# Kernel tuning notes

Measured on AMD Instinct MI355X. Metric: run time of the kernel, lower is better.

The kernel has to match this reference:

```python
import jax, jax.numpy as jnp
import numpy as np

V, D, H, L, E, DH, K, PMAX = 50257, 128, 4, 4, 8, 512, 2, 256
B, T = 8, 256


def setup_inputs() -> dict:
    key = jax.random.key(0)
    ks = jax.random.split(key, 10)
    s = 0.02
    def n(k, shape):
        return jax.random.normal(k, shape, jnp.float32) * s
    return dict(
        idx=jax.random.randint(ks[0], (B, T), 0, V),
        tok_emb=n(ks[1], (V, D)),
        pos_emb=n(ks[2], (PMAX, D)),
        ln1_g=jnp.ones((L, D), jnp.float32), ln1_b=jnp.zeros((L, D), jnp.float32),
        in_w=n(ks[3], (L, 3 * D, D)), in_b=jnp.zeros((L, 3 * D), jnp.float32),
        out_w=n(ks[4], (L, D, D)), out_b=jnp.zeros((L, D), jnp.float32),
        ln2_g=jnp.ones((L, D), jnp.float32), ln2_b=jnp.zeros((L, D), jnp.float32),
        gate_w=n(ks[5], (L, E, D)),
        w1=n(ks[6], (L, E, DH, D)),
        w2=n(ks[7], (L, E, D, DH)),
        lnf_g=jnp.ones((D,), jnp.float32), lnf_b=jnp.zeros((D,), jnp.float32),
        lm_w=n(ks[8], (V, D)),
    )


def _ln(x, g, b):
    mu = x.mean(-1, keepdims=True)
    var = jnp.var(x, -1, keepdims=True)
    return (x - mu) / jnp.sqrt(var + 1e-5) * g + b


def _moe(x, gw, w1, w2):
    # x: [N, D]; top-2 sparse MoE, computed densely per expert then combined.
    logits = x @ gw.T                              # [N, E]
    probs = jax.nn.softmax(logits, -1)
    topw, topi = jax.lax.top_k(probs, K)           # [N, K]
    topw = topw / topw.sum(-1, keepdims=True)
    we = (topw[..., None] * jax.nn.one_hot(topi, E, dtype=x.dtype)).sum(1)  # [N, E]
    h = jax.nn.silu(jnp.einsum('nd,ehd->neh', x, w1))   # [N, E, DH]
    y = jnp.einsum('neh,edh->ned', h, w2)               # [N, E, D]
    return jnp.einsum('ned,ne->nd', y, we)


def reference(idx, tok_emb, pos_emb, ln1_g, ln1_b, in_w, in_b, out_w, out_b,
              ln2_g, ln2_b, gate_w, w1, w2, lnf_g, lnf_b, lm_w):
    b, t = idx.shape
    x = tok_emb[idx] + pos_emb[:t]                 # [B, T, D]
    dh = D // H
    scale = 1.0 / np.sqrt(dh)
    for l in range(L):
        xl = _ln(x, ln1_g[l], ln1_b[l])
        qkv = xl @ in_w[l].T + in_b[l]
        q, k, v = jnp.split(qkv, 3, -1)
        q = q.reshape(b, t, H, dh)
        k = k.reshape(b, t, H, dh)
        v = v.reshape(b, t, H, dh)
        att = jax.nn.softmax(jnp.einsum('bqhd,bkhd->bhqk', q, k) * scale, -1)
        o = jnp.einsum('bhqk,bkhd->bqhd', att, v).reshape(b, t, D)
        x = x + o @ out_w[l].T + out_b[l]
        x2 = _ln(x, ln2_g[l], ln2_b[l]).reshape(b * t, D)
        x = x + _moe(x2, gate_w[l], w1[l], w2[l]).reshape(b, t, D)
    return _ln(x, lnf_g, lnf_b) @ lm_w.T           # [B, T, V]
```

## Files before the change

kernel.cpp:

```cpp
#include <hip/hip_runtime.h>
#include <math.h>

#define NTOK 2048
#define DD   128
#define NHEAD 4
#define DHEAD 32
#define NLAYER 4
#define NEXP 8
#define DHID 512
#define NVOCAB 50257
#define VPAD  50304
#define SEQ   256
#define NBATCH 8

typedef __attribute__((ext_vector_type(8))) short short8v;
typedef __attribute__((ext_vector_type(4))) float f32x4;

__device__ __forceinline__ unsigned short nm_bf16r(float f) {
  unsigned u = __float_as_uint(f);
  u += 0x7fffu + ((u >> 16) & 1u);
  return (unsigned short)(u >> 16);
}

__device__ __forceinline__ float nm_silu(float a) {
// ... 8 lines not shown
  float sx = 0.f, sy = 0.f, sz = 0.f, sw = 0.f;
#pragma unroll 16
  for (int k = 0; k < N4; ++k) {
    float4 av = a4[k], wv = w4[k];
    sx = fmaf(av.x, wv.x, sx);
    sy = fmaf(av.y, wv.y, sy);
    sz = fmaf(av.z, wv.z, sz);
    sw = fmaf(av.w, wv.w, sw);
  }
  return (sx + sy) + (sz + sw);
}

__global__ void nm_embed_ln(const int* __restrict__ idx, const float* __restrict__ tok,
                            const float* __restrict__ pos, const float* __restrict__ g,
                            const float* __restrict__ b, float* __restrict__ x,
                            float* __restrict__ xl) {
  int n = blockIdx.x, lane = threadIdx.x;
  int t = idx[n];
  float v0 = tok[(size_t)t * DD + lane]      + pos[(n % SEQ) * DD + lane];
  float v1 = tok[(size_t)t * DD + lane + 64] + pos[(n % SEQ) * DD + lane + 64];
  x[n * DD + lane]      = v0;
  x[n * DD + lane + 64] = v1;
  float s = v0 + v1;
#pragma unroll
  for (int o = 32; o > 0; o >>= 1) s += __shfl_xor(s, o, 64);
  float mu = s * (1.f / 128.f);
  float d0 = v0 - mu, d1 = v1 - mu;
  float q = d0 * d0 + d1 * d1;
#pragma unroll
  for (int o = 32; o > 0; o >>= 1) q += __shfl_xor(q, o, 64);
  float rstd = rsqrtf(q * (1.f / 128.f) + 1e-5f);
  xl[n * DD + lane]      = d0 * rstd * g[lane]      + b[lane];
  xl[n * DD + lane + 64] = d1 * rstd * g[lane + 64] + b[lane + 64];
}

__global__ void nm_ln(const float* __restrict__ in, const float* __restrict__ g,
                      const float* __restrict__ b, float* __restrict__ out) {
  int n = blockIdx.x, lane = threadIdx.x;
  float v0 = in[n * DD + lane], v1 = in[n * DD + lane + 64];
  float s = v0 + v1;
#pragma unroll
  for (int o = 32; o > 0; o >>= 1) s += __shfl_xor(s, o, 64);
  float mu = s * (1.f / 128.f);
  float d0 = v0 - mu, d1 = v1 - mu;
  float q = d0 * d0 + d1 * d1;
#pragma unroll
  for (int o = 32; o > 0; o >>= 1) q += __shfl_xor(q, o, 64);
  float rstd = rsqrtf(q * (1.f / 128.f) + 1e-5f);
  out[n * DD + lane]      = d0 * rstd * g[lane]      + b[lane];
  out[n * DD + lane + 64] = d1 * rstd * g[lane + 64] + b[lane + 64];
}

__global__ void nm_combine_ln(const float* __restrict__ yb, const int* __restrict__ posm,
                              const float* __restrict__ topw, float* __restrict__ x,
                              const float* __restrict__ g, const float* __restrict__ b,
                              float* __restrict__ xl, unsigned short* __restrict__ xb) {
  int n = blockIdx.x, lane = threadIdx.x;
  float w0 = topw[2 * n], w1 = topw[2 * n + 1];
  int p0 = posm[2 * n], p1 = posm[2 * n + 1];
  float v0 = x[n * DD + lane]      + w0 * yb[(size_t)p0 * DD + lane]
                                   + w1 * yb[(size_t)p1 * DD + lane];
  float v1 = x[n * DD + lane + 64] + w0 * yb[(size_t)p0 * DD + lane + 64]
                                   + w1 * yb[(size_t)p1 * DD + lane + 64];
  x[n * DD + lane]      = v0;
  x[n * DD + lane + 64] = v1;
  float s = v0 + v1;
#pragma unroll
  for (int o = 32; o > 0; o >>= 1) s += __shfl_xor(s, o, 64);
  float mu = s * (1.f / 128.f);
  float d0 = v0 - mu, d1 = v1 - mu;
  float q = d0 * d0 + d1 * d1;
#pragma unroll
  for (int o = 32; o > 0; o >>= 1) q += __shfl_xor(q, o, 64);
  float rstd = rsqrtf(q * (1.f / 128.f) + 1e-5f);
  float o0 = d0 * rstd * g[lane]      + b[lane];
  float o1 = d1 * rstd * g[lane + 64] + b[lane + 64];
  xl[n * DD + lane]      = o0;
  xl[n * DD + lane + 64] = o1;
  if (xb) {
    xb[n * DD + lane]      = nm_bf16r(o0);
    xb[n * DD + lane + 64] = nm_bf16r(o1);
  }
}

template<int F>
__global__ __launch_bounds__(256) void nm_gemm(
    const float* __restrict__ A, const float* __restrict__ B,
    float* __restrict__ C, const float* __restrict__ bias,
    int M, int N, int K,
    const int* __restrict__ list, const int* __restrict__ cnt,
    const int* __restrict__ off) {
  constexpr bool GA = F & 1, SI = F & 2, BI = F & 4, RE = F & 8, GR = F & 16;
  __shared__ __align__(16) float As[64][68];
  __shared__ __align__(16) float Bs[64][68];
  int tid = threadIdx.x;
  int n0 = blockIdx.x * 64, m0 = blockIdx.y * 64;
  int Mloc = M, o = 0;
  const float* Bb = B;
  if constexpr (GR) {
    int e = blockIdx.z;
    Mloc = cnt[e];
    if (m0 >= Mloc) return;
    o = off[e];
    Bb = B + (size_t)e * (size_t)N * K;
  }
  int tm = tid & 15, tn = tid >> 4;
  float acc[4][4] = {};
  for (int kc = 0; kc < K; kc += 64) {
#pragma unroll
    for (int i = 0; i < 4; ++i) {
      int f = tid + 256 * i;
      int r = f >> 4, c4 = f & 15;
      int mi = m0 + r;
      if (mi >= Mloc) mi = m0;
      const float* ar;
      if constexpr (GA) ar = A + (size_t)(list[o + mi] >> 1) * K;
      else              ar = A + (size_t)(o + mi) * K;
      float4 v = *(const float4*)(ar + kc + c4 * 4);
      int k = c4 * 4;
      As[k][r] = v.x; As[k + 1][r] = v.y; As[k + 2][r] = v.z; As[k + 3][r] = v.w;
    }
#pragma unroll
    for (int i = 0; i < 4; ++i) {
      int f = tid + 256 * i;
      int r = f >> 4, c4 = f & 15;
      const float* br = Bb + (size_t)(n0 + r) * K + kc + c4 * 4;
      float4 v = *(const float4*)br;
      int k = c4 * 4;
      Bs[k][r] = v.x; Bs[k + 1][r] = v.y; Bs[k + 2][r] = v.z; Bs[k + 3][r] = v.w;
    }
    __syncthreads();
#pragma unroll 16
    for (int k = 0; k < 64; ++k) {
      float4 a = *(const float4*)&As[k][tm * 4];
      float4 b = *(const float4*)&Bs[k][tn * 4];
      acc[0][0] = fmaf(a.x, b.x, acc[0][0]); acc[0][1] = fmaf(a.x, b.y, acc[0][1]);
      acc[0][2] = fmaf(a.x, b.z, acc[0][2]); acc[0][3] = fmaf(a.x, b.w, acc[0][3]);
      acc[1][0] = fmaf(a.y, b.x, acc[1][0]); acc[1][1] = fmaf(a.y, b.y, acc[1][1]);
      acc[1][2] = fmaf(a.y, b.z, acc[1][2]); acc[1][3] = fmaf(a.y, b.w, acc[1][3]);
      acc[2][0] = fmaf(a.z, b.x, acc[2][0]); acc[2][1] = fmaf(a.z, b.y, acc[2][1]);
      acc[2][2] = fmaf(a.z, b.z, acc[2][2]); acc[2][3] = fmaf(a.z, b.w, acc[2][3]);
      acc[3][0] = fmaf(a.w, b.x, acc[3][0]); acc[3][1] = fmaf(a.w, b.y, acc[3][1]);
      acc[3][2] = fmaf(a.w, b.z, acc[3][2]); acc[3][3] = fmaf(a.w, b.w, acc[3][3]);
    }
    __syncthreads();
  }
  float4 bv = {0.f, 0.f, 0.f, 0.f};
  if constexpr (BI) bv = *(const float4*)(bias + n0 + tn * 4);
#pragma unroll
  for (int i = 0; i < 4; ++i) {
    int mi = m0 + tm * 4 + i;
    if (GR && mi >= Mloc) continue;
    float* cr = C + (size_t)(o + mi) * N + n0 + tn * 4;
    float r0 = acc[i][0], r1 = acc[i][1], r2 = acc[i][2], r3 = acc[i][3];
    if constexpr (BI) { r0 += bv.x; r1 += bv.y; r2 += bv.z; r3 += bv.w; }
    if constexpr (SI) { r0 = nm_silu(r0); r1 = nm_silu(r1); r2 = nm_silu(r2); r3 = nm_silu(r3); }
    if constexpr (RE) { r0 += cr[0]; r1 += cr[1]; r2 += cr[2]; r3 += cr[3]; }
    float4 st = {r0, r1, r2, r3};
    *(float4*)cr = st;
  }
}

__global__ __launch_bounds__(256) void nm_oplng(
    const float* __restrict__ ao, const float* __restrict__ w,
    const float* __restrict__ bias, float* __restrict__ x,
    const float* __restrict__ g, const float* __restrict__ b,
    float* __restrict__ xl, const float* __restrict__ gw,
    int* __restrict__ topi, float* __restrict__ topw, int* __restrict__ cnt) {
  __shared__ __align__(16) float As[64][36];
  __shared__ __align__(16) float Bs[64][132];
  __shared__ float Ls[32][9];
  int tid = threadIdx.x;
  int m0 = blockIdx.x * 32;
  int tm = tid >> 5, tn = tid & 31;
  float acc[4][4] = {};
  for (int kc = 0; kc < DD; kc += 64) {
#pragma unroll
    for (int i = 0; i < 2; ++i) {
      int ch = tid + 256 * i, r = ch >> 4, c4 = ch & 15;
      float4 v = *(const float4*)(ao + (size_t)(m0 + r) * DD + kc + c4 * 4);
      int k = c4 * 4;
      As[k][r] = v.x; As[k + 1][r] = v.y; As[k + 2][r] = v.z; As[k + 3][r] = v.w;
    }
#pragma unroll
    for (int i = 0; i < 8; ++i) {
      int ch = tid + 256 * i, r = ch >> 4, c4 = ch & 15;
      float4 v = *(const float4*)(w + (size_t)r * DD + kc + c4 * 4);
      int k = c4 * 4;
// ... 76 lines not shown
#pragma unroll
    for (int e = 1; e < NEXP; ++e) if (gl[e] > gl[i0]) i0 = e;
    int i1 = (i0 == 0) ? 1 : 0;
#pragma unroll
    for (int e = 0; e < NEXP; ++e) { if (e != i0 && gl[e] > gl[i1]) i1 = e; }
    float p1 = __expf(gl[i1] - gl[i0]);
    float inv = 1.f / (1.f + p1);
    int n = m0 + grow;
    topi[2 * n] = i0; topi[2 * n + 1] = i1;
    topw[2 * n] = inv; topw[2 * n + 1] = p1 * inv;
    atomicAdd(cnt + i0, 1);
    atomicAdd(cnt + i1, 1);
  }
}

__global__ __launch_bounds__(256) void nm_attn2(const float* __restrict__ qkv,
                                                float* __restrict__ o) {
  __shared__ __align__(16) float Ks[SEQ][DHEAD];
  __shared__ __align__(16) float Vs[SEQ][DHEAD];
  __shared__ float mbuf[32][9], sbuf[32][9];
  __shared__ __align__(16) float accbuf[32][36];
  int bh = blockIdx.x;
  int b = bh >> 2, h = bh & 3;
  int qt = blockIdx.y;
  int tid = threadIdx.x;
  const float* base = qkv + (size_t)b * SEQ * 384;
  for (int f = tid; f < SEQ * 8; f += 256) {
    int t = f >> 3, c4 = f & 7;
    float4 kv = *(const float4*)(base + (size_t)t * 384 + 128 + h * DHEAD + c4 * 4);
    float4 vv = *(const float4*)(base + (size_t)t * 384 + 256 + h * DHEAD + c4 * 4);
    *(float4*)&Ks[t][c4 * 4] = kv;
    *(float4*)&Vs[t][c4 * 4] = vv;
  }
  __syncthreads();
  int q = tid & 31, slot = tid >> 5;
  int tq = qt * 32 + q;
  float qv[DHEAD];
  const float4* q4 = (const float4*)(base + (size_t)tq * 384 + h * DHEAD);
#pragma unroll
  for (int k = 0; k < 8; ++k) {
    float4 v = q4[k];
    qv[4*k] = v.x; qv[4*k+1] = v.y; qv[4*k+2] = v.z; qv[4*k+3] = v.w;
  }
  float m = -1e30f, s = 0.f, acc[DHEAD];
#pragma unroll
  for (int d = 0; d < DHEAD; ++d) acc[d] = 0.f;
  const float scale = 0.17677669529663687f;
  int j0 = slot * 32;
  for (int jj = 0; jj < 32; ++jj) {
    int j = j0 + jj;
    const float4* kr = (const float4*)Ks[j];
    float sc = 0.f;
#pragma unroll
    for (int k = 0; k < 8; ++k) {
      float4 v = kr[k];
      sc += qv[4*k]*v.x + qv[4*k+1]*v.y + qv[4*k+2]*v.z + qv[4*k+3]*v.w;
    }
    sc *= scale;
    float mn = fmaxf(m, sc);
    float f = __expf(m - mn), p = __expf(sc - mn);
    s = s * f + p;
    const float4* vr = (const float4*)Vs[j];
#pragma unroll
    for (int k = 0; k < 8; ++k) {
      float4 v = vr[k];
      acc[4*k]   = acc[4*k]  * f + p * v.x;
      acc[4*k+1] = acc[4*k+1]* f + p * v.y;
      acc[4*k+2] = acc[4*k+2]* f + p * v.z;
      acc[4*k+3] = acc[4*k+3]* f + p * v.w;
    }
    m = mn;
  }
  mbuf[q][slot] = m;
  sbuf[q][slot] = s;
  __syncthreads();
  float M = mbuf[q][0];
#pragma unroll
  for (int t = 1; t < 8; ++t) M = fmaxf(M, mbuf[q][t]);
  float S = 0.f;
#pragma unroll
  for (int t = 0; t < 8; ++t) S += sbuf[q][t] * __expf(mbuf[q][t] - M);
  float w = __expf(m - M);
#pragma unroll
  for (int d = 0; d < DHEAD; ++d) acc[d] *= w;
#pragma unroll
  for (int p = 0; p < 8; ++p) {
    if (slot == p) {
      if (p == 0) {
#pragma unroll
        for (int d = 0; d < DHEAD; ++d) accbuf[q][d] = acc[d];
      } else {
#pragma unroll
        for (int d = 0; d < DHEAD; ++d) accbuf[q][d] += acc[d];
      }
    }
    __syncthreads();
  }
  if (slot == 0) sbuf[q][8] = 1.f / S;
  __syncthreads();
  int q2 = tid >> 3, c4 = tid & 7;
  float inv = sbuf[q2][8];
  float4 v = *(const float4*)&accbuf[q2][c4 * 4];
  v.x *= inv; v.y *= inv; v.z *= inv; v.w *= inv;
  *(float4*)(o + (size_t)(b * SEQ + qt * 32 + q2) * DD + h * DHEAD + c4 * 4) = v;
}

__global__ void nm_route(const int* __restrict__ topi, const int* __restrict__ cnt,
                         int* __restrict__ off, int* __restrict__ list,
                         int* __restrict__ posm) {
  __shared__ int lcur[NEXP];
  int tid = threadIdx.x;
  if (tid < NEXP) {
    int o = 0;
    for (int e = 0; e < tid; ++e) o += cnt[e];
    lcur[tid] = o;
    off[tid] = o;
  }
  __syncthreads();
  for (int t = tid; t < 2 * NTOK; t += 1024) {
    int e = topi[t];
    int p = atomicAdd(&lcur[e], 1);
    list[p] = t;
    posm[t] = p;
  }
}

__global__ void nm_zero(int* __restrict__ p, int n) {
  int i = blockIdx.x * 64 + threadIdx.x;
  if (i < n) p[i] = 0;
}

__global__ void nm_moe(const float* __restrict__ x2, const float* __restrict__ gw,
                       const float* __restrict__ w1, const float* __restrict__ w2,
                       float* __restrict__ x) {
  __shared__ __align__(16) float xs[DD];
  __shared__ __align__(16) float hs[DHID];
  __shared__ float gl[NEXP];
  __shared__ int   ei[2];
  __shared__ float ew[2];
  int n = blockIdx.x, tid = threadIdx.x;
  if (tid < DD) xs[tid] = x2[n * DD + tid];
  __syncthreads();
  if (tid < NEXP) gl[tid] = nm_dotv<32>(xs, gw + (size_t)tid * DD);
  __syncthreads();
// ... 14 lines not shown
    float wt = ew[t2];
    const float* w1e = w1 + (size_t)e * DHID * DD;
#pragma unroll
    for (int jj = 0; jj < 2; ++jj) {
      int j = tid + jj * 256;
      float a = nm_dotv<32>(xs, w1e + (size_t)j * DD);
      hs[j] = nm_silu(a);
    }
    __syncthreads();
    if (tid < DD) yacc += wt * nm_dotv<128>(hs, w2 + ((size_t)e * DD + tid) * DHID);
    __syncthreads();
  }
  if (tid < DD) x[n * DD + tid] += yacc;
}

__global__ void nm_cvt_w(const float* __restrict__ in, unsigned short* __restrict__ ob) {
  size_t i = (size_t)blockIdx.x * 256 + threadIdx.x;
  const size_t n = (size_t)NVOCAB * DD;
  ob[i] = (i < n) ? nm_bf16r(in[i]) : (unsigned short)0;
}

__device__ __forceinline__ short8v nm_cvt8(const float* p) {
  const float4* p4 = (const float4*)p;
  float4 a = p4[0], b = p4[1];
  short8v r;
  r[0] = (short)nm_bf16r(a.x); r[1] = (short)nm_bf16r(a.y);
  r[2] = (short)nm_bf16r(a.z); r[3] = (short)nm_bf16r(a.w);
  r[4] = (short)nm_bf16r(b.x); r[5] = (short)nm_bf16r(b.y);
  r[6] = (short)nm_bf16r(b.z); r[7] = (short)nm_bf16r(b.w);
  return r;
}

__global__ __launch_bounds__(256) void nm_lmhead2(
    const unsigned short* __restrict__ xfb, const unsigned short* __restrict__ lmwb,
    float* __restrict__ out) {
  __shared__ unsigned short Ab[128 * 128];
  __shared__ unsigned short Bb[128 * 128];
  int tid = threadIdx.x;
  int row0 = blockIdx.y * 128, col0 = blockIdx.x * 128;
#pragma unroll
  for (int i = 0; i < 8; ++i) {
    int ch = tid + i * 256;
    int r = ch >> 4, s = ch & 15;
    int sg = s ^ (r & 7);
    *(short8v*)&Ab[r * 128 + s * 8] =
        *(const short8v*)(xfb + (size_t)(row0 + r) * DD + sg * 8);
    *(short8v*)&Bb[r * 128 + s * 8] =
        *(const short8v*)(lmwb + (size_t)(col0 + r) * DD + sg * 8);
  }
  __syncthreads();
  int wave = tid >> 6, lane = tid & 63;
  int wr = wave >> 1, wc = wave & 1;
  int lr = lane & 15, hk = lane >> 4;
  f32x4 acc[4][4] = {};
#pragma unroll
  for (int ks = 0; ks < 4; ++ks) {
    int sg = ks * 4 + hk;
    int sx = (sg ^ (lr & 7)) * 8;
    short8v a[4], b[4];
#pragma unroll
    for (int i = 0; i < 4; ++i)
      a[i] = *(const short8v*)&Ab[(wr * 64 + i * 16 + lr) * 128 + sx];
#pragma unroll
    for (int j = 0; j < 4; ++j)
      b[j] = *(const short8v*)&Bb[(wc * 64 + j * 16 + lr) * 128 + sx];
#pragma unroll
    for (int i = 0; i < 4; ++i)
#pragma unroll
      for (int j = 0; j < 4; ++j)
        acc[i][j] = __builtin_amdgcn_mfma_f32_16x16x32_bf16(a[i], b[j], acc[i][j], 0, 0, 0);
  }
  int cr = (lane >> 4) * 4;
#pragma unroll
  for (int j = 0; j < 4; ++j) {
    int c = col0 + wc * 64 + j * 16 + (lane & 15);
    if (c < NVOCAB) {
#pragma unroll
      for (int i = 0; i < 4; ++i)
#pragma unroll
        for (int r = 0; r < 4; ++r)
          out[(size_t)(row0 + wr * 64 + i * 16 + cr + r) * NVOCAB + c] = acc[i][j][r];
    }
  }
}

__global__ __launch_bounds__(256) void nm_lmhead_f32(
    const float* __restrict__ xf, const float* __restrict__ lmw,
    float* __restrict__ out) {
  int wave = threadIdx.x >> 6, lane = threadIdx.x & 63;
  int wr = wave >> 1, wc = wave & 1;
  int row0 = blockIdx.y * 128 + wr * 64;
  int col0 = blockIdx.x * 128 + wc * 64;
  int lr = lane & 15, lk = (lane >> 4) * 8;
  f32x4 acc[4][4] = {};
#pragma unroll
  for (int ks = 0; ks < 4; ++ks) {
    int kb = ks * 32 + lk;
    short8v a[4], b[4];
#pragma unroll
    for (int i = 0; i < 4; ++i)
// ... 13 lines not shown
    for (int i = 0; i < 4; ++i)
#pragma unroll
      for (int j = 0; j < 4; ++j)
        acc[i][j] = __builtin_amdgcn_mfma_f32_16x16x32_bf16(a[i], b[j], acc[i][j], 0, 0, 0);
  }
  int cr = (lane >> 4) * 4;
#pragma unroll
  for (int j = 0; j < 4; ++j) {
    int c = col0 + j * 16 + (lane & 15);
    if (c < NVOCAB) {
#pragma unroll
      for (int i = 0; i < 4; ++i)
#pragma unroll
        for (int r = 0; r < 4; ++r)
          out[(size_t)(row0 + i * 16 + cr + r) * NVOCAB + c] = acc[i][j][r];
    }
  }
}

extern "C" void kernel_launch(void* const* d_in, const int* in_sizes, int n_in,
                              void* d_out, int out_size, void* d_ws, size_t ws_size,
                              hipStream_t stream) {
  const int*   idx   = (const int*)  d_in[0];
  const float* tok   = (const float*)d_in[1];
  const float* pos   = (const float*)d_in[2];
  const float* ln1g  = (const float*)d_in[3];
  const float* ln1b  = (const float*)d_in[4];
  const float* inw   = (const float*)d_in[5];
  const float* inb   = (const float*)d_in[6];
  const float* outw  = (const float*)d_in[7];
// ... 2 lines not shown
  const float* ln2b  = (const float*)d_in[10];
  const float* gatew = (const float*)d_in[11];
  const float* w1    = (const float*)d_in[12];
  const float* w2    = (const float*)d_in[13];
  const float* lnfg  = (const float*)d_in[14];
  const float* lnfb  = (const float*)d_in[15];
  const float* lmw   = (const float*)d_in[16];
  float* out = (float*)d_out;

  float* ws   = (float*)d_ws;
  float* x    = ws;
  float* xl   = x    + NTOK * DD;
  float* qkv  = xl   + NTOK * DD;
  float* ao   = qkv  + NTOK * 384;
  float* topw = ao   + NTOK * DD;
  int*   topi = (int*)(topw + 2 * NTOK);
  int*   list = topi + 2 * NTOK;
  int*   posm = list + 2 * NTOK;
  int*   cnt  = posm + 2 * NTOK;
  int*   offs = cnt  + NLAYER * NEXP;
  float* H    = (float*)(offs + NLAYER * NEXP);
  float* yb   = H    + 2 * NTOK * DHID;
  unsigned short* xfb  = (unsigned short*)(yb + 2 * NTOK * DD);
  unsigned short* lmwb = xfb + NTOK * DD;

  const size_t moe_bytes = (size_t)((char*)xfb - (char*)d_ws);
  const size_t pre_bytes = moe_bytes + ((size_t)NTOK * DD + (size_t)VPAD * DD) * 2;
  const bool moe_ok = (ws_size >= moe_bytes);
  const bool pre = (ws_size >= pre_bytes);

  nm_embed_ln<<<NTOK, 64, 0, stream>>>(idx, tok, pos, ln1g, ln1b, x, xl);
  if (moe_ok) nm_zero<<<(NLAYER * NEXP + 63) / 64, 64, 0, stream>>>(cnt, NLAYER * NEXP);
  if (pre) nm_cvt_w<<<VPAD * DD / 256, 256, 0, stream>>>(lmw, lmwb);

  for (int l = 0; l < NLAYER; ++l) {
    nm_gemm<4><<<dim3(384 / 64, NTOK / 64), 256, 0, stream>>>(
        xl, inw + (size_t)l * 384 * DD, qkv, inb + (size_t)l * 384,
        NTOK, 384, DD, nullptr, nullptr, nullptr);
    nm_attn2<<<dim3(NBATCH * NHEAD, SEQ / 32), 256, 0, stream>>>(qkv, ao);
    nm_oplng<<<NTOK / 32, 256, 0, stream>>>(
        ao, outw + (size_t)l * DD * DD, outb + (size_t)l * DD, x,
        ln2g + l * DD, ln2b + l * DD, xl, gatew + (size_t)l * NEXP * DD,
        topi, topw, cnt + l * NEXP);

    const float* gN = (l < NLAYER - 1) ? ln1g + (l + 1) * DD : lnfg;
    const float* bN = (l < NLAYER - 1) ? ln1b + (l + 1) * DD : lnfb;
    if (moe_ok) {
      int* cnt_l = cnt + l * NEXP;
      int* off_l = offs + l * NEXP;
      const float* w1l = w1 + (size_t)l * NEXP * DHID * DD;
      const float* w2l = w2 + (size_t)l * NEXP * DD * DHID;
      nm_route<<<1, 1024, 0, stream>>>(topi, cnt_l, off_l, list, posm);
      nm_gemm<19><<<dim3(DHID / 64, 2 * NTOK / 64, NEXP), 256, 0, stream>>>(
          xl, w1l, H, nullptr, 0, DHID, DD, list, cnt_l, off_l);
      nm_gemm<16><<<dim3(DD / 64, 2 * NTOK / 64, NEXP), 256, 0, stream>>>(
          H, w2l, yb, nullptr, 0, DD, DHID, nullptr, cnt_l, off_l);
      nm_combine_ln<<<NTOK, 64, 0, stream>>>(
          yb, posm, topw, x, gN, bN, xl,
          (l == NLAYER - 1 && pre) ? xfb : (unsigned short*)nullptr);
    } else {
      nm_moe<<<NTOK, 256, 0, stream>>>(xl, gatew + (size_t)l * NEXP * DD,
                                       w1 + (size_t)l * NEXP * DHID * DD,
                                       w2 + (size_t)l * NEXP * DD * DHID, x);
      nm_ln<<<NTOK, 64, 0, stream>>>(x, gN, bN, xl);
    }
  }

  if (pre) {
    nm_lmhead2<<<dim3(VPAD / 128, NTOK / 128), 256, 0, stream>>>(xfb, lmwb, out);
  } else {
    nm_lmhead_f32<<<dim3(VPAD / 128, NTOK / 128), 256, 0, stream>>>(xl, lmw, out);
  }
}
```

Measured before the change: 848.9 us.

## Fuse all transformer layers into one persistent megakernel with grid barriers

Replaces the per-layer chain of launches (QKV GEMM, attention, out-proj+LN+gate, routing, two grouped expert GEMMs, combine+LN) with a single persistent kernel of 256 blocks. The stages are separated by a software global barrier built on atomics, and block-local shared memory is a union reused across stages. The grouped GEMM tile is widened to 128 rows per block, and the fallback path is restructured. This removes many kernel-launch gaps and tail effects. In exchange it relies on all 256 blocks being co-resident for the spin barrier, and each stage runs with a fixed grid size that may underuse the device.

```diff
diff --git a/kernel.cpp b/kernel.cpp
--- a/kernel.cpp
+++ b/kernel.cpp
@@ -46,7 +46,7 @@
 __global__ void nm_embed_ln(const int* __restrict__ idx, const float* __restrict__ tok,
                             const float* __restrict__ pos, const float* __restrict__ g,
                             const float* __restrict__ b, float* __restrict__ x,
-                            float* __restrict__ xl) {
+                            float* __restrict__ xlf, unsigned short* __restrict__ xlb) {
   int n = blockIdx.x, lane = threadIdx.x;
   int t = idx[n];
   float v0 = tok[(size_t)t * DD + lane]      + pos[(n % SEQ) * DD + lane];
@@ -62,8 +62,10 @@
 #pragma unroll
   for (int o = 32; o > 0; o >>= 1) q += __shfl_xor(q, o, 64);
   float rstd = rsqrtf(q * (1.f / 128.f) + 1e-5f);
-  xl[n * DD + lane]      = d0 * rstd * g[lane]      + b[lane];
-  xl[n * DD + lane + 64] = d1 * rstd * g[lane + 64] + b[lane + 64];
+  float o0 = d0 * rstd * g[lane]      + b[lane];
+  float o1 = d1 * rstd * g[lane + 64] + b[lane + 64];
+  if (xlf) { xlf[n * DD + lane] = o0; xlf[n * DD + lane + 64] = o1; }
+  if (xlb) { xlb[n * DD + lane] = nm_bf16r(o0); xlb[n * DD + lane + 64] = nm_bf16r(o1); }
 }
 
 __global__ void nm_ln(const float* __restrict__ in, const float* __restrict__ g,
@@ -83,64 +85,50 @@
   out[n * DD + lane + 64] = d1 * rstd * g[lane + 64] + b[lane + 64];
 }
 
-__global__ void nm_combine_ln(const float* __restrict__ yb, const int* __restrict__ posm,
-                              const float* __restrict__ topw, float* __restrict__ x,
-                              const float* __restrict__ g, const float* __restrict__ b,
-                              float* __restrict__ xl, unsigned short* __restrict__ xb) {
-  int n = blockIdx.x, lane = threadIdx.x;
-  float w0 = topw[2 * n], w1 = topw[2 * n + 1];
-  int p0 = posm[2 * n], p1 = posm[2 * n + 1];
-  float v0 = x[n * DD + lane]      + w0 * yb[(size_t)p0 * DD + lane]
-                                   + w1 * yb[(size_t)p1 * DD + lane];
-  float v1 = x[n * DD + lane + 64] + w0 * yb[(size_t)p0 * DD + lane + 64]
-                                   + w1 * yb[(size_t)p1 * DD + lane + 64];
-  x[n * DD + lane]      = v0;
-  x[n * DD + lane + 64] = v1;
-  float s = v0 + v1;
-#pragma unroll
-  for (int o = 32; o > 0; o >>= 1) s += __shfl_xor(s, o, 64);
-  float mu = s * (1.f / 128.f);
-  float d0 = v0 - mu, d1 = v1 - mu;
-  float q = d0 * d0 + d1 * d1;
-#pragma unroll
-  for (int o = 32; o > 0; o >>= 1) q += __shfl_xor(q, o, 64);
-  float rstd = rsqrtf(q * (1.f / 128.f) + 1e-5f);
-  float o0 = d0 * rstd * g[lane]      + b[lane];
-  float o1 = d1 * rstd * g[lane + 64] + b[lane + 64];
-  xl[n * DD + lane]      = o0;
-  xl[n * DD + lane + 64] = o1;
-  if (xb) {
-    xb[n * DD + lane]      = nm_bf16r(o0);
-    xb[n * DD + lane + 64] = nm_bf16r(o1);
-  }
-}
-
-template<int F>
-__global__ __launch_bounds__(256) void nm_gemm(
-    const float* __restrict__ A, const float* __restrict__ B,
+__global__ void nm_zero(int* __restrict__ p, int n) {
+  int i = blockIdx.x * 128 + threadIdx.x;
+  if (i < n) p[i] = 0;
+}
+
+__global__ void nm_cvt_w(const float* __restrict__ in, unsigned short* __restrict__ ob) {
+  size_t i = (size_t)blockIdx.x * 256 + threadIdx.x;
+  const size_t n = (size_t)NVOCAB * DD;
+  ob[i] = (i < n) ? nm_bf16r(in[i]) : (unsigned short)0;
+}
+
+struct __align__(16) SMemG { float As[64][132]; float Bs[64][68]; };
+struct __align__(16) SMemA {
+  float Ks[SEQ][DHEAD]; float Vs[SEQ][DHEAD];
+  float mb[32][9]; float sb[32][9]; float ab[32][36];
+};
+struct __align__(16) SMemO { float As[64][36]; float Bs[64][132]; float Ls[32][9]; };
+struct __align__(16) SMemR { int lcur[NEXP]; };
+union SMem { SMemG g; SMemA a; SMemO o; SMemR r; };
+
+__device__ __forceinline__ void nm_gbar(int* __restrict__ gbar, int target) {
+  __syncthreads();
+  if (threadIdx.x == 0) {
+    __threadfence();
+    atomicAdd(gbar, 1);
+    while (atomicAdd(gbar, 0) < target) __builtin_amdgcn_s_sleep(2);
+    __threadfence();
+  }
+  __syncthreads();
+}
+
+template<bool GA, bool SI, bool BI>
+__device__ void dev_gemm2(SMem& sm, int n0, int m0,
+    const float* __restrict__ A, const float* __restrict__ Bb,
     float* __restrict__ C, const float* __restrict__ bias,
-    int M, int N, int K,
-    const int* __restrict__ list, const int* __restrict__ cnt,
-    const int* __restrict__ off) {
-  constexpr bool GA = F & 1, SI = F & 2, BI = F & 4, RE = F & 8, GR = F & 16;
-  __shared__ __align__(16) float As[64][68];
-  __shared__ __align__(16) float Bs[64][68];
+    int Mloc, int o, int N, int K, const int* __restrict__ list) {
+  auto& As = sm.g.As;
+  auto& Bs = sm.g.Bs;
   int tid = threadIdx.x;
-  int n0 = blockIdx.x * 64, m0 = blockIdx.y * 64;
-  int Mloc = M, o = 0;
-  const float* Bb = B;
-  if constexpr (GR) {
-    int e = blockIdx.z;
-    Mloc = cnt[e];
-    if (m0 >= Mloc) return;
-    o = off[e];
-    Bb = B + (size_t)e * (size_t)N * K;
-  }
   int tm = tid & 15, tn = tid >> 4;
-  float acc[4][4] = {};
+  float acc[8][4] = {};
   for (int kc = 0; kc < K; kc += 64) {
 #pragma unroll
-    for (int i = 0; i < 4; ++i) {
+    for (int i = 0; i < 8; ++i) {
       int f = tid + 256 * i;
       int r = f >> 4, c4 = f & 15;
       int mi = m0 + r;
@@ -164,46 +152,142 @@
     __syncthreads();
 #pragma unroll 16
     for (int k = 0; k < 64; ++k) {
-      float4 a = *(const float4*)&As[k][tm * 4];
+      float4 a0 = *(const float4*)&As[k][tm * 4];
+      float4 a1 = *(const float4*)&As[k][64 + tm * 4];
       float4 b = *(const float4*)&Bs[k][tn * 4];
-      acc[0][0] = fmaf(a.x, b.x, acc[0][0]); acc[0][1] = fmaf(a.x, b.y, acc[0][1]);
-      acc[0][2] = fmaf(a.x, b.z, acc[0][2]); acc[0][3] = fmaf(a.x, b.w, acc[0][3]);
-      acc[1][0] = fmaf(a.y, b.x, acc[1][0]); acc[1][1] = fmaf(a.y, b.y, acc[1][1]);
-      acc[1][2] = fmaf(a.y, b.z, acc[1][2]); acc[1][3] = fmaf(a.y, b.w, acc[1][3]);
-      acc[2][0] = fmaf(a.z, b.x, acc[2][0]); acc[2][1] = fmaf(a.z, b.y, acc[2][1]);
-      acc[2][2] = fmaf(a.z, b.z, acc[2][2]); acc[2][3] = fmaf(a.z, b.w, acc[2][3]);
-      acc[3][0] = fmaf(a.w, b.x, acc[3][0]); acc[3][1] = fmaf(a.w, b.y, acc[3][1]);
-      acc[3][2] = fmaf(a.w, b.z, acc[3][2]); acc[3][3] = fmaf(a.w, b.w, acc[3][3]);
+      acc[0][0] = fmaf(a0.x, b.x, acc[0][0]); acc[0][1] = fmaf(a0.x, b.y, acc[0][1]);
+      acc[0][2] = fmaf(a0.x, b.z, acc[0][2]); acc[0][3] = fmaf(a0.x, b.w, acc[0][3]);
+      acc[1][0] = fmaf(a0.y, b.x, acc[1][0]); acc[1][1] = fmaf(a0.y, b.y, acc[1][1]);
+      acc[1][2] = fmaf(a0.y, b.z, acc[1][2]); acc[1][3] = fmaf(a0.y, b.w, acc[1][3]);
+      acc[2][0] = fmaf(a0.z, b.x, acc[2][0]); acc[2][1] = fmaf(a0.z, b.y, acc[2][1]);
+      acc[2][2] = fmaf(a0.z, b.z, acc[2][2]); acc[2][3] = fmaf(a0.z, b.w, acc[2][3]);
+      acc[3][0] = fmaf(a0.w, b.x, acc[3][0]); acc[3][1] = fmaf(a0.w, b.y, acc[3][1]);
+      acc[3][2] = fmaf(a0.w, b.z, acc[3][2]); acc[3][3] = fmaf(a0.w, b.w, acc[3][3]);
+      acc[4][0] = fmaf(a1.x, b.x, acc[4][0]); acc[4][1] = fmaf(a1.x, b.y, acc[4][1]);
+      acc[4][2] = fmaf(a1.x, b.z, acc[4][2]); acc[4][3] = fmaf(a1.x, b.w, acc[4][3]);
+      acc[5][0] = fmaf(a1.y, b.x, acc[5][0]); acc[5][1] = fmaf(a1.y, b.y, acc[5][1]);
+      acc[5][2] = fmaf(a1.y, b.z, acc[5][2]); acc[5][3] = fmaf(a1.y, b.w, acc[5][3]);
+      acc[6][0] = fmaf(a1.z, b.x, acc[6][0]); acc[6][1] = fmaf(a1.z, b.y, acc[6][1]);
+      acc[6][2] = fmaf(a1.z, b.z, acc[6][2]); acc[6][3] = fmaf(a1.z, b.w, acc[6][3]);
+      acc[7][0] = fmaf(a1.w, b.x, acc[7][0]); acc[7][1] = fmaf(a1.w, b.y, acc[7][1]);
+      acc[7][2] = fmaf(a1.w, b.z, acc[7][2]); acc[7][3] = fmaf(a1.w, b.w, acc[7][3]);
     }
     __syncthreads();
   }
   float4 bv = {0.f, 0.f, 0.f, 0.f};
   if constexpr (BI) bv = *(const float4*)(bias + n0 + tn * 4);
 #pragma unroll
-  for (int i = 0; i < 4; ++i) {
-    int mi = m0 + tm * 4 + i;
-    if (GR && mi >= Mloc) continue;
-    float* cr = C + (size_t)(o + mi) * N + n0 + tn * 4;
-    float r0 = acc[i][0], r1 = acc[i][1], r2 = acc[i][2], r3 = acc[i][3];
-    if constexpr (BI) { r0 += bv.x; r1 += bv.y; r2 += bv.z; r3 += bv.w; }
-    if constexpr (SI) { r0 = nm_silu(r0); r1 = nm_silu(r1); r2 = nm_silu(r2); r3 = nm_silu(r3); }
-    if constexpr (RE) { r0 += cr[0]; r1 += cr[1]; r2 += cr[2]; r3 += cr[3]; }
-    float4 st = {r0, r1, r2, r3};
-    *(float4*)cr = st;
-  }
-}
-
-__global__ __launch_bounds__(256) void nm_oplng(
-    const float* __restrict__ ao, const float* __restrict__ w,
-    const float* __restrict__ bias, float* __restrict__ x,
-    const float* __restrict__ g, const float* __restrict__ b,
-    float* __restrict__ xl, const float* __restrict__ gw,
-    int* __restrict__ topi, float* __restrict__ topw, int* __restrict__ cnt) {
-  __shared__ __align__(16) float As[64][36];
-  __shared__ __align__(16) float Bs[64][132];
-  __shared__ float Ls[32][9];
+  for (int g = 0; g < 2; ++g) {
+#pragma unroll
+    for (int i = 0; i < 4; ++i) {
+      int row = m0 + g * 64 + tm * 4 + i;
+      if (row >= Mloc) continue;
+      float* cr = C + (size_t)(o + row) * N + n0 + tn * 4;
+      float r0 = acc[g * 4 + i][0], r1 = acc[g * 4 + i][1];
+      float r2 = acc[g * 4 + i][2], r3 = acc[g * 4 + i][3];
+      if constexpr (BI) { r0 += bv.x; r1 += bv.y; r2 += bv.z; r3 += bv.w; }
+      if constexpr (SI) { r0 = nm_silu(r0); r1 = nm_silu(r1); r2 = nm_silu(r2); r3 = nm_silu(r3); }
+      float4 st = {r0, r1, r2, r3};
+      *(float4*)cr = st;
+    }
+  }
+}
+
+__device__ void dev_attn(SMem& sm, int tile, const float* __restrict__ qkv,
+                         float* __restrict__ o) {
+  int bh = tile >> 3, qt = tile & 7;
+  int b = bh >> 2, h = bh & 3;
   int tid = threadIdx.x;
-  int m0 = blockIdx.x * 32;
+  const float* base = qkv + (size_t)b * SEQ * 384;
+  for (int f = tid; f < SEQ * 8; f += 256) {
+    int t = f >> 3, c4 = f & 7;
+    float4 kv = *(const float4*)(base + (size_t)t * 384 + 128 + h * DHEAD + c4 * 4);
+    float4 vv = *(const float4*)(base + (size_t)t * 384 + 256 + h * DHEAD + c4 * 4);
+    *(float4*)&sm.a.Ks[t][c4 * 4] = kv;
+    *(float4*)&sm.a.Vs[t][c4 * 4] = vv;
+  }
+  __syncthreads();
+  int q = tid & 31, slot = tid >> 5;
+  int tq = qt * 32 + q;
+  float qv[DHEAD];
+  const float4* q4 = (const float4*)(base + (size_t)tq * 384 + h * DHEAD);
+#pragma unroll
+  for (int k = 0; k < 8; ++k) {
+    float4 v = q4[k];
+    qv[4*k] = v.x; qv[4*k+1] = v.y; qv[4*k+2] = v.z; qv[4*k+3] = v.w;
+  }
+  float m = -1e30f, s = 0.f, acc[DHEAD];
+#pragma unroll
+  for (int d = 0; d < DHEAD; ++d) acc[d] = 0.f;
+  const float scale = 0.17677669529663687f;
+  int j0 = slot * 32;
+  for (int jj = 0; jj < 32; ++jj) {
+    int j = j0 + jj;
+    const float4* kr = (const float4*)sm.a.Ks[j];
+    float sc = 0.f;
+#pragma unroll
+    for (int k = 0; k < 8; ++k) {
+      float4 v = kr[k];
+      sc += qv[4*k]*v.x + qv[4*k+1]*v.y + qv[4*k+2]*v.z + qv[4*k+3]*v.w;
+    }
+    sc *= scale;
+    float mn = fmaxf(m, sc);
+    float f = __expf(m - mn), p = __expf(sc - mn);
+    s = s * f + p;
+    const float4* vr = (const float4*)sm.a.Vs[j];
+#pragma unroll
+    for (int k = 0; k < 8; ++k) {
+      float4 v = vr[k];
+      acc[4*k]   = acc[4*k]  * f + p * v.x;
+      acc[4*k+1] = acc[4*k+1]* f + p * v.y;
+      acc[4*k+2] = acc[4*k+2]* f + p * v.z;
+      acc[4*k+3] = acc[4*k+3]* f + p * v.w;
+    }
+    m = mn;
+  }
+  sm.a.mb[q][slot] = m;
+  sm.a.sb[q][slot] = s;
+  __syncthreads();
+  float M = sm.a.mb[q][0];
+#pragma unroll
+  for (int t = 1; t < 8; ++t) M = fmaxf(M, sm.a.mb[q][t]);
+  float S = 0.f;
+#pragma unroll
+  for (int t = 0; t < 8; ++t) S += sm.a.sb[q][t] * __expf(sm.a.mb[q][t] - M);
+  float w = __expf(m - M);
+#pragma unroll
+  for (int d = 0; d < DHEAD; ++d) acc[d] *= w;
+#pragma unroll
+  for (int p = 0; p < 8; ++p) {
+    if (slot == p) {
+      if (p == 0) {
+#pragma unroll
+        for (int d = 0; d < DHEAD; ++d) sm.a.ab[q][d] = acc[d];
+      } else {
+#pragma unroll
+        for (int d = 0; d < DHEAD; ++d) sm.a.ab[q][d] += acc[d];
+      }
+    }
+    __syncthreads();
+  }
+  if (slot == 0) sm.a.sb[q][8] = 1.f / S;
+  __syncthreads();
+  int q2 = tid >> 3, c4 = tid & 7;
+  float inv = sm.a.sb[q2][8];
+  float4 v = *(const float4*)&sm.a.ab[q2][c4 * 4];
+  v.x *= inv; v.y *= inv; v.z *= inv; v.w *= inv;
+  *(float4*)(o + (size_t)(b * SEQ + qt * 32 + q2) * DD + h * DHEAD + c4 * 4) = v;
+}
+
+__device__ void dev_oplng(SMem& sm, int m0, const float* __restrict__ ao,
+    const float* __restrict__ w, const float* __restrict__ bias, float* __restrict__ x,
+    const float* __restrict__ g, const float* __restrict__ b, float* __restrict__ xl,
+    const float* __restrict__ gw, int* __restrict__ topi, float* __restrict__ topw,
+    int* __restrict__ cnt) {
+  auto& As = sm.o.As;
+  auto& Bs = sm.o.Bs;
+  auto& Ls = sm.o.Ls;
+  int tid = threadIdx.x;
   int tm = tid >> 5, tn = tid & 31;
   float acc[4][4] = {};
   for (int kc = 0; kc < DD; kc += 64) {
@@ -310,120 +394,150 @@
   }
 }
 
-__global__ __launch_bounds__(256) void nm_attn2(const float* __restrict__ qkv,
-                                                float* __restrict__ o) {
-  __shared__ __align__(16) float Ks[SEQ][DHEAD];
-  __shared__ __align__(16) float Vs[SEQ][DHEAD];
-  __shared__ float mbuf[32][9], sbuf[32][9];
-  __shared__ __align__(16) float accbuf[32][36];
-  int bh = blockIdx.x;
-  int b = bh >> 2, h = bh & 3;
-  int qt = blockIdx.y;
-  int tid = threadIdx.x;
-  const float* base = qkv + (size_t)b * SEQ * 384;
-  for (int f = tid; f < SEQ * 8; f += 256) {
-    int t = f >> 3, c4 = f & 7;
-    float4 kv = *(const float4*)(base + (size_t)t * 384 + 128 + h * DHEAD + c4 * 4);
-    float4 vv = *(const float4*)(base + (size_t)t * 384 + 256 + h * DHEAD + c4 * 4);
-    *(float4*)&Ks[t][c4 * 4] = kv;
-    *(float4*)&Vs[t][c4 * 4] = vv;
-  }
-  __syncthreads();
-  int q = tid & 31, slot = tid >> 5;
-  int tq = qt * 32 + q;
-  float qv[DHEAD];
-  const float4* q4 = (const float4*)(base + (size_t)tq * 384 + h * DHEAD);
-#pragma unroll
-  for (int k = 0; k < 8; ++k) {
-    float4 v = q4[k];
-    qv[4*k] = v.x; qv[4*k+1] = v.y; qv[4*k+2] = v.z; qv[4*k+3] = v.w;
-  }
-  float m = -1e30f, s = 0.f, acc[DHEAD];
-#pragma unroll
-  for (int d = 0; d < DHEAD; ++d) acc[d] = 0.f;
-  const float scale = 0.17677669529663687f;
-  int j0 = slot * 32;
-  for (int jj = 0; jj < 32; ++jj) {
-    int j = j0 + jj;
-    const float4* kr = (const float4*)Ks[j];
-    float sc = 0.f;
-#pragma unroll
-    for (int k = 0; k < 8; ++k) {
-      float4 v = kr[k];
-      sc += qv[4*k]*v.x + qv[4*k+1]*v.y + qv[4*k+2]*v.z + qv[4*k+3]*v.w;
-    }
-    sc *= scale;
-    float mn = fmaxf(m, sc);
-    float f = __expf(m - mn), p = __expf(sc - mn);
-    s = s * f + p;
-    const float4* vr = (const float4*)Vs[j];
-#pragma unroll
-    for (int k = 0; k < 8; ++k) {
-      float4 v = vr[k];
-      acc[4*k]   = acc[4*k]  * f + p * v.x;
-      acc[4*k+1] = acc[4*k+1]* f + p * v.y;
-      acc[4*k+2] = acc[4*k+2]* f + p * v.z;
-      acc[4*k+3] = acc[4*k+3]* f + p * v.w;
-    }
-    m = mn;
-  }
-  mbuf[q][slot] = m;
-  sbuf[q][slot] = s;
-  __syncthreads();
-  float M = mbuf[q][0];
-#pragma unroll
-  for (int t = 1; t < 8; ++t) M = fmaxf(M, mbuf[q][t]);
-  float S = 0.f;
-#pragma unroll
-  for (int t = 0; t < 8; ++t) S += sbuf[q][t] * __expf(mbuf[q][t] - M);
-  float w = __expf(m - M);
-#pragma unroll
-  for (int d = 0; d < DHEAD; ++d) acc[d] *= w;
-#pragma unroll
-  for (int p = 0; p < 8; ++p) {
-    if (slot == p) {
-      if (p == 0) {
-#pragma unroll
-        for (int d = 0; d < DHEAD; ++d) accbuf[q][d] = acc[d];
-      } else {
-#pragma unroll
-        for (int d = 0; d < DHEAD; ++d) accbuf[q][d] += acc[d];
-      }
-    }
-    __syncthreads();
-  }
-  if (slot == 0) sbuf[q][8] = 1.f / S;
-  __syncthreads();
-  int q2 = tid >> 3, c4 = tid & 7;
-  float inv = sbuf[q2][8];
-  float4 v = *(const float4*)&accbuf[q2][c4 * 4];
-  v.x *= inv; v.y *= inv; v.z *= inv; v.w *= inv;
-  *(float4*)(o + (size_t)(b * SEQ + qt * 32 + q2) * DD + h * DHEAD + c4 * 4) = v;
-}
-
-__global__ void nm_route(const int* __restrict__ topi, const int* __restrict__ cnt,
-                         int* __restrict__ off, int* __restrict__ list,
-                         int* __restrict__ posm) {
-  __shared__ int lcur[NEXP];
+__device__ void dev_route(SMem& sm, const int* __restrict__ topi,
+                          const int* __restrict__ cnt, int* __restrict__ off,
+                          int* __restrict__ list, int* __restrict__ posm) {
   int tid = threadIdx.x;
   if (tid < NEXP) {
     int o = 0;
     for (int e = 0; e < tid; ++e) o += cnt[e];
-    lcur[tid] = o;
+    sm.r.lcur[tid] = o;
     off[tid] = o;
   }
   __syncthreads();
-  for (int t = tid; t < 2 * NTOK; t += 1024) {
+  for (int t = tid; t < 2 * NTOK; t += 256) {
     int e = topi[t];
-    int p = atomicAdd(&lcur[e], 1);
+    int p = atomicAdd(&sm.r.lcur[e], 1);
     list[p] = t;
     posm[t] = p;
   }
 }
 
-__global__ void nm_zero(int* __restrict__ p, int n) {
-  int i = blockIdx.x * 64 + threadIdx.x;
-  if (i < n) p[i] = 0;
+__device__ void dev_combine(int bid, const float* __restrict__ yb,
+    const int* __restrict__ posm, const float* __restrict__ topw,
+    float* __restrict__ x, const float* __restrict__ g, const float* __restrict__ b,
+    float* __restrict__ xl, unsigned short* __restrict__ xb) {
+  int wv = threadIdx.x >> 6, lane = threadIdx.x & 63;
+  for (int n = bid * 4 + wv; n < NTOK; n += 1024) {
+    float w0 = topw[2 * n], w1 = topw[2 * n + 1];
+    int p0 = posm[2 * n], p1 = posm[2 * n + 1];
+    float v0 = x[n * DD + lane]      + w0 * yb[(size_t)p0 * DD + lane]
+                                     + w1 * yb[(size_t)p1 * DD + lane];
+    float v1 = x[n * DD + lane + 64] + w0 * yb[(size_t)p0 * DD + lane + 64]
+                                     + w1 * yb[(size_t)p1 * DD + lane + 64];
+    x[n * DD + lane]      = v0;
+    x[n * DD + lane + 64] = v1;
+    float s = v0 + v1;
+#pragma unroll
+    for (int o = 32; o > 0; o >>= 1) s += __shfl_xor(s, o, 64);
+    float mu = s * (1.f / 128.f);
+    float d0 = v0 - mu, d1 = v1 - mu;
+    float q = d0 * d0 + d1 * d1;
+#pragma unroll
+    for (int o = 32; o > 0; o >>= 1) q += __shfl_xor(q, o, 64);
+    float rstd = rsqrtf(q * (1.f / 128.f) + 1e-5f);
+    float o0 = d0 * rstd * g[lane]      + b[lane];
+    float o1 = d1 * rstd * g[lane + 64] + b[lane + 64];
+    xl[n * DD + lane]      = o0;
+    xl[n * DD + lane + 64] = o1;
+    if (xb) {
+      xb[n * DD + lane]      = nm_bf16r(o0);
+      xb[n * DD + lane + 64] = nm_bf16r(o1);
+    }
+  }
+}
+
+__global__ __launch_bounds__(256) void nm_mega(
+    const float* __restrict__ inw, const float* __restrict__ inb,
+    const float* __restrict__ outw, const float* __restrict__ outb,
+    const float* __restrict__ ln1g, const float* __restrict__ ln1b,
+    const float* __restrict__ ln2g, const float* __restrict__ ln2b,
+    const float* __restrict__ gatew, const float* __restrict__ w1,
+    const float* __restrict__ w2, const float* __restrict__ lnfg,
+    const float* __restrict__ lnfb,
+    float* __restrict__ x, float* __restrict__ xl, float* __restrict__ qkv,
+    float* __restrict__ ao, float* __restrict__ topw, float* __restrict__ H,
+    float* __restrict__ yb, int* __restrict__ topi, int* __restrict__ list,
+    int* __restrict__ posm, int* __restrict__ cnt, int* __restrict__ offs,
+    int* __restrict__ gbar, unsigned short* __restrict__ xfb) {
+  __shared__ SMem sm;
+  int bid = blockIdx.x;
+  int nb = 0;
+  for (int l = 0; l < NLAYER; ++l) {
+    const float* inwl  = inw  + (size_t)l * 384 * DD;
+    const float* inbl  = inb  + (size_t)l * 384;
+    const float* outwl = outw + (size_t)l * DD * DD;
+    const float* outbl = outb + (size_t)l * DD;
+    const float* gwl   = gatew + (size_t)l * NEXP * DD;
+    const float* w1l   = w1 + (size_t)l * NEXP * DHID * DD;
+    const float* w2l   = w2 + (size_t)l * NEXP * DD * DHID;
+    int* cnt_l = cnt + l * NEXP;
+    int* off_l = offs + l * NEXP;
+    const float* gN = (l < NLAYER - 1) ? ln1g + (l + 1) * DD : lnfg;
+    const float* bN = (l < NLAYER - 1) ? ln1b + (l + 1) * DD : lnfb;
+
+    if (bid < 96)
+      dev_gemm2<false, false, true>(sm, (bid % 6) * 64, (bid / 6) * 128,
+          xl, inwl, qkv, inbl, NTOK, 0, 384, DD, nullptr);
+    nm_gbar(gbar, ++nb * 256);
+
+    dev_attn(sm, bid, qkv, ao);
+    nm_gbar(gbar, ++nb * 256);
+
+    if (bid < 64)
+      dev_oplng(sm, bid * 32, ao, outwl, outbl, x, ln2g + l * DD, ln2b + l * DD,
+                xl, gwl, topi, topw, cnt_l);
+    nm_gbar(gbar, ++nb * 256);
+
+    if (bid == 0) dev_route(sm, topi, cnt_l, off_l, list, posm);
+    nm_gbar(gbar, ++nb * 256);
+
+    for (int vt = bid; vt < 2048; vt += 256) {
+      int e = vt >> 8, rem = vt & 255;
+      int m0 = (rem >> 3) * 128, n0 = (rem & 7) * 64;
+      int c = cnt_l[e];
+      if (m0 < c)
+        dev_gemm2<true, true, false>(sm, n0, m0, xl,
+            w1l + (size_t)e * DHID * DD, H, nullptr, c, off_l[e], DHID, DD, list);
+    }
+    nm_gbar(gbar, ++nb * 256);
+
+    for (int vt = bid; vt < 512; vt += 256) {
+      int e = vt >> 6, rem = vt & 63;
+      int m0 = (rem >> 1) * 128, n0 = (rem & 1) * 64;
+      int c = cnt_l[e];
+      if (m0 < c)
+        dev_gemm2<false, false, false>(sm, n0, m0, H,
+            w2l + (size_t)e * DD * DHID, yb, nullptr, c, off_l[e], DD, DHID, nullptr);
+    }
+    nm_gbar(gbar, ++nb * 256);
+
+    dev_combine(bid, yb, posm, topw, x, gN, bN, xl,
+                (l == NLAYER - 1) ? xfb : (unsigned short*)nullptr);
+    nm_gbar(gbar, ++nb * 256);
+  }
+}
+
+__global__ void nm_qkv(const float* __restrict__ xl, const float* __restrict__ w,
+                       const float* __restrict__ bias, float* __restrict__ qkv) {
+  __shared__ __align__(16) float xs[DD];
+  int n = blockIdx.x, tid = threadIdx.x;
+  xs[tid] = xl[n * DD + tid];
+  __syncthreads();
+#pragma unroll
+  for (int jj = 0; jj < 3; ++jj) {
+    int j = tid + jj * 128;
+    qkv[(size_t)n * 384 + j] = nm_dotv<32>(xs, w + (size_t)j * DD) + bias[j];
+  }
+}
+
+__global__ void nm_outproj(const float* __restrict__ ao, const float* __restrict__ w,
+                           const float* __restrict__ bias, float* __restrict__ x) {
+  __shared__ __align__(16) float os[DD];
+  int n = blockIdx.x, tid = threadIdx.x;
+  os[tid] = ao[n * DD + tid];
+  __syncthreads();
+  x[n * DD + tid] += nm_dotv<32>(os, w + (size_t)tid * DD) + bias[tid];
 }
 
 __global__ void nm_moe(const float* __restrict__ x2, const float* __restrict__ gw,
@@ -468,10 +582,11 @@
   if (tid < DD) x[n * DD + tid] += yacc;
 }
 
-__global__ void nm_cvt_w(const float* __restrict__ in, unsigned short* __restrict__ ob) {
-  size_t i = (size_t)blockIdx.x * 256 + threadIdx.x;
-  const size_t n = (size_t)NVOCAB * DD;
-  ob[i] = (i < n) ? nm_bf16r(in[i]) : (unsigned short)0;
+__global__ __launch_bounds__(256) void nm_attn2(const float* __restrict__ qkv,
+                                                float* __restrict__ o) {
+  __shared__ SMem sm;
+  int tile = blockIdx.x * 8 + blockIdx.y;
+  dev_attn(sm, tile, qkv, o);
 }
 
 __device__ __forceinline__ short8v nm_cvt8(const float* p) {
@@ -485,59 +600,6 @@
   return r;
 }
 
-__global__ __launch_bounds__(256) void nm_lmhead2(
-    const unsigned short* __restrict__ xfb, const unsigned short* __restrict__ lmwb,
-    float* __restrict__ out) {
-  __shared__ unsigned short Ab[128 * 128];
-  __shared__ unsigned short Bb[128 * 128];
-  int tid = threadIdx.x;
-  int row0 = blockIdx.y * 128, col0 = blockIdx.x * 128;
-#pragma unroll
-  for (int i = 0; i < 8; ++i) {
-    int ch = tid + i * 256;
-    int r = ch >> 4, s = ch & 15;
-    int sg = s ^ (r & 7);
-    *(short8v*)&Ab[r * 128 + s * 8] =
-        *(const short8v*)(xfb + (size_t)(row0 + r) * DD + sg * 8);
-    *(short8v*)&Bb[r * 128 + s * 8] =
-        *(const short8v*)(lmwb + (size_t)(col0 + r) * DD + sg * 8);
-  }
-  __syncthreads();
-  int wave = tid >> 6, lane = tid & 63;
-  int wr = wave >> 1, wc = wave & 1;
-  int lr = lane & 15, hk = lane >> 4;
-  f32x4 acc[4][4] = {};
-#pragma unroll
-  for (int ks = 0; ks < 4; ++ks) {
-    int sg = ks * 4 + hk;
-    int sx = (sg ^ (lr & 7)) * 8;
-    short8v a[4], b[4];
-#pragma unroll
-    for (int i = 0; i < 4; ++i)
-      a[i] = *(const short8v*)&Ab[(wr * 64 + i * 16 + lr) * 128 + sx];
-#pragma unroll
-    for (int j = 0; j < 4; ++j)
-      b[j] = *(const short8v*)&Bb[(wc * 64 + j * 16 + lr) * 128 + sx];
-#pragma unroll
-    for (int i = 0; i < 4; ++i)
-#pragma unroll
-      for (int j = 0; j < 4; ++j)
-        acc[i][j] = __builtin_amdgcn_mfma_f32_16x16x32_bf16(a[i], b[j], acc[i][j], 0, 0, 0);
-  }
-  int cr = (lane >> 4) * 4;
-#pragma unroll
-  for (int j = 0; j < 4; ++j) {
-    int c = col0 + wc * 64 + j * 16 + (lane & 15);
-    if (c < NVOCAB) {
-#pragma unroll
-      for (int i = 0; i < 4; ++i)
-#pragma unroll
-        for (int r = 0; r < 4; ++r)
-          out[(size_t)(row0 + wr * 64 + i * 16 + cr + r) * NVOCAB + c] = acc[i][j][r];
-    }
-  }
-}
-
 __global__ __launch_bounds__(256) void nm_lmhead_f32(
     const float* __restrict__ xf, const float* __restrict__ lmw,
     float* __restrict__ out) {
@@ -581,6 +643,59 @@
 #pragma unroll
         for (int r = 0; r < 4; ++r)
           out[(size_t)(row0 + i * 16 + cr + r) * NVOCAB + c] = acc[i][j][r];
+    }
+  }
+}
+
+__global__ __launch_bounds__(256) void nm_lmhead2(
+    const unsigned short* __restrict__ xfb, const unsigned short* __restrict__ lmwb,
+    float* __restrict__ out) {
+  __shared__ unsigned short Ab[128 * 128];
+  __shared__ unsigned short Bb[128 * 128];
+  int tid = threadIdx.x;
+  int row0 = blockIdx.y * 128, col0 = blockIdx.x * 128;
+#pragma unroll
+  for (int i = 0; i < 8; ++i) {
+    int ch = tid + i * 256;
+    int r = ch >> 4, s = ch & 15;
+    int sg = s ^ (r & 7);
+    *(short8v*)&Ab[r * 128 + s * 8] =
+        *(const short8v*)(xfb + (size_t)(row0 + r) * DD + sg * 8);
+    *(short8v*)&Bb[r * 128 + s * 8] =
+        *(const short8v*)(lmwb + (size_t)(col0 + r) * DD + sg * 8);
+  }
+  __syncthreads();
+  int wave = tid >> 6, lane = tid & 63;
+  int wr = wave >> 1, wc = wave & 1;
+  int lr = lane & 15, hk = lane >> 4;
+  f32x4 acc[4][4] = {};
+#pragma unroll
+  for (int ks = 0; ks < 4; ++ks) {
+    int sg = ks * 4 + hk;
+    int sx = (sg ^ (lr & 7)) * 8;
+    short8v a[4], b[4];
+#pragma unroll
+    for (int i = 0; i < 4; ++i)
+      a[i] = *(const short8v*)&Ab[(wr * 64 + i * 16 + lr) * 128 + sx];
+#pragma unroll
+    for (int j = 0; j < 4; ++j)
+      b[j] = *(const short8v*)&Bb[(wc * 64 + j * 16 + lr) * 128 + sx];
+#pragma unroll
+    for (int i = 0; i < 4; ++i)
+#pragma unroll
+      for (int j = 0; j < 4; ++j)
+        acc[i][j] = __builtin_amdgcn_mfma_f32_16x16x32_bf16(a[i], b[j], acc[i][j], 0, 0, 0);
+  }
+  int cr = (lane >> 4) * 4;
+#pragma unroll
+  for (int j = 0; j < 4; ++j) {
+    int c = col0 + wc * 64 + j * 16 + (lane & 15);
+    if (c < NVOCAB) {
+#pragma unroll
+      for (int i = 0; i < 4; ++i)
+#pragma unroll
+        for (int r = 0; r < 4; ++r)
+          out[(size_t)(row0 + wr * 64 + i * 16 + cr + r) * NVOCAB + c] = acc[i][j][r];
     }
   }
 }
@@ -613,61 +728,43 @@
   float* qkv  = xl   + NTOK * DD;
   float* ao   = qkv  + NTOK * 384;
   float* topw = ao   + NTOK * DD;
-  int*   topi = (int*)(topw + 2 * NTOK);
+  float* H    = topw + 2 * NTOK;
+  float* yb   = H    + 2 * NTOK * DHID;
+  int*   topi = (int*)(yb + 2 * NTOK * DD);
   int*   list = topi + 2 * NTOK;
   int*   posm = list + 2 * NTOK;
   int*   cnt  = posm + 2 * NTOK;
   int*   offs = cnt  + NLAYER * NEXP;
-  float* H    = (float*)(offs + NLAYER * NEXP);
-  float* yb   = H    + 2 * NTOK * DHID;
-  unsigned short* xfb  = (unsigned short*)(yb + 2 * NTOK * DD);
+  int*   gbar = offs + NLAYER * NEXP;
+  unsigned short* xfb  = (unsigned short*)(gbar + 8);
   unsigned short* lmwb = xfb + NTOK * DD;
-
-  const size_t moe_bytes = (size_t)((char*)xfb - (char*)d_ws);
-  const size_t pre_bytes = moe_bytes + ((size_t)NTOK * DD + (size_t)VPAD * DD) * 2;
-  const bool moe_ok = (ws_size >= moe_bytes);
-  const bool pre = (ws_size >= pre_bytes);
-
-  nm_embed_ln<<<NTOK, 64, 0, stream>>>(idx, tok, pos, ln1g, ln1b, x, xl);
-  if (moe_ok) nm_zero<<<(NLAYER * NEXP + 63) / 64, 64, 0, stream>>>(cnt, NLAYER * NEXP);
-  if (pre) nm_cvt_w<<<VPAD * DD / 256, 256, 0, stream>>>(lmw, lmwb);
-
-  for (int l = 0; l < NLAYER; ++l) {
-    nm_gemm<4><<<dim3(384 / 64, NTOK / 64), 256, 0, stream>>>(
-        xl, inw + (size_t)l * 384 * DD, qkv, inb + (size_t)l * 384,
-        NTOK, 384, DD, nullptr, nullptr, nullptr);
-    nm_attn2<<<dim3(NBATCH * NHEAD, SEQ / 32), 256, 0, stream>>>(qkv, ao);
-    nm_oplng<<<NTOK / 32, 256, 0, stream>>>(
-        ao, outw + (size_t)l * DD * DD, outb + (size_t)l * DD, x,
-        ln2g + l * DD, ln2b + l * DD, xl, gatew + (size_t)l * NEXP * DD,
-        topi, topw, cnt + l * NEXP);
-
-    const float* gN = (l < NLAYER - 1) ? ln1g + (l + 1) * DD : lnfg;
-    const float* bN = (l < NLAYER - 1) ? ln1b + (l + 1) * DD : lnfb;
-    if (moe_ok) {
-      int* cnt_l = cnt + l * NEXP;
-      int* off_l = offs + l * NEXP;
-      const float* w1l = w1 + (size_t)l * NEXP * DHID * DD;
-      const float* w2l = w2 + (size_t)l * NEXP * DD * DHID;
-      nm_route<<<1, 1024, 0, stream>>>(topi, cnt_l, off_l, list, posm);
-      nm_gemm<19><<<dim3(DHID / 64, 2 * NTOK / 64, NEXP), 256, 0, stream>>>(
-          xl, w1l, H, nullptr, 0, DHID, DD, list, cnt_l, off_l);
-      nm_gemm<16><<<dim3(DD / 64, 2 * NTOK / 64, NEXP), 256, 0, stream>>>(
-          H, w2l, yb, nullptr, 0, DD, DHID, nullptr, cnt_l, off_l);
-      nm_combine_ln<<<NTOK, 64, 0, stream>>>(
-          yb, posm, topw, x, gN, bN, xl,
-          (l == NLAYER - 1 && pre) ? xfb : (unsigned short*)nullptr);
-    } else {
+  const size_t need = (size_t)((char*)(lmwb + (size_t)VPAD * DD) - (char*)d_ws);
+  const bool pre = (ws_size >= need);
+
+  if (pre) {
+    nm_cvt_w<<<VPAD * DD / 256, 256, 0, stream>>>(lmw, lmwb);
+    nm_zero<<<1, 128, 0, stream>>>(cnt, 72);
+    nm_embed_ln<<<NTOK, 64, 0, stream>>>(idx, tok, pos, ln1g, ln1b, x, xl, nullptr);
+    nm_mega<<<256, 256, 0, stream>>>(
+        inw, inb, outw, outb, ln1g, ln1b, ln2g, ln2b, gatew, w1, w2, lnfg, lnfb,
+        x, xl, qkv, ao, topw, H, yb, topi, list, posm, cnt, offs, gbar, xfb);
+    nm_lmhead2<<<dim3(VPAD / 128, NTOK / 128), 256, 0, stream>>>(xfb, lmwb, out);
+  } else {
+    nm_embed_ln<<<NTOK, 64, 0, stream>>>(idx, tok, pos, ln1g, ln1b, x, xl, nullptr);
+    for (int l = 0; l < NLAYER; ++l) {
+      nm_qkv<<<NTOK, 128, 0, stream>>>(xl, inw + (size_t)l * 384 * DD,
+                                       inb + (size_t)l * 384, qkv);
+      nm_attn2<<<dim3(32, 8), 256, 0, stream>>>(qkv, ao);
+      nm_outproj<<<NTOK, 128, 0, stream>>>(ao, outw + (size_t)l * DD * DD,
+                                           outb + (size_t)l * DD, x);
+      nm_ln<<<NTOK, 64, 0, stream>>>(x, ln2g + l * DD, ln2b + l * DD, xl);
       nm_moe<<<NTOK, 256, 0, stream>>>(xl, gatew + (size_t)l * NEXP * DD,
                                        w1 + (size_t)l * NEXP * DHID * DD,
                                        w2 + (size_t)l * NEXP * DD * DHID, x);
+      const float* gN = (l < NLAYER - 1) ? ln1g + (l + 1) * DD : lnfg;
+      const float* bN = (l < NLAYER - 1) ? ln1b + (l + 1) * DD : lnfb;
       nm_ln<<<NTOK, 64, 0, stream>>>(x, gN, bN, xl);
     }
-  }
-
-  if (pre) {
-    nm_lmhead2<<<dim3(VPAD / 128, NTOK / 128), 256, 0, stream>>>(xfb, lmwb, out);
-  } else {
     nm_lmhead_f32<<<dim3(VPAD / 128, NTOK / 128), 256, 0, stream>>>(xl, lmw, out);
   }
 }
```

Result: slower. 2.018 ms (+137.7%).
